# Performance work log

Measured on AMD Instinct MI355X. Metric: run time of the kernel, lower is better.

The kernel has to match this reference:

```python
import math
import jax, jax.numpy as jnp
import numpy as np

# ---- module hyperparameters (from init_kwargs) ----
N_DELTA, N_THETA, N_GAMMA = 32, 64, 256
N_TOTAL = N_DELTA + N_THETA + N_GAMMA  # 352
N_DIMS = 1024
BATCH = 4096
N_STEPS = 32
DT = 0.01
COUPLING = 2.0
PAC = 0.3
EPS = 1e-6
TWO_PI = 2.0 * math.pi


def setup_inputs() -> dict:
    key = jax.random.key(0)
    k0, k1, k2 = jax.random.split(key, 3)
    x = jax.random.normal(k0, (BATCH, N_DIMS), dtype=jnp.float32)
    # xavier_uniform with gain=0.5 for Linear(n_dims, n_total, bias=False)
    bound = 0.5 * math.sqrt(6.0 / (N_DIMS + N_TOTAL))
    W_phase = jax.random.uniform(k1, (N_TOTAL, N_DIMS), jnp.float32, -bound, bound)
    W_amp = jax.random.uniform(k2, (N_TOTAL, N_DIMS), jnp.float32, -bound, bound)
    # natural angular frequencies per band: delta ~2Hz, theta ~6Hz, gamma ~40Hz
    omega = jnp.concatenate([
        jnp.full((N_DELTA,), TWO_PI * 2.0, jnp.float32),
        jnp.full((N_THETA,), TWO_PI * 6.0, jnp.float32),
        jnp.full((N_GAMMA,), TWO_PI * 40.0, jnp.float32),
    ])
    # block-diagonal intra-band Kuramoto coupling, K_ij = coupling_strength / n_band
    Kn = np.zeros((N_TOTAL, N_TOTAL), dtype=np.float32)
    o = 0
    for nb in (N_DELTA, N_THETA, N_GAMMA):
        Kn[o:o + nb, o:o + nb] = COUPLING / nb
        o += nb
    K = jnp.asarray(Kn)
    return {"x": x, "W_phase": W_phase, "W_amp": W_amp, "omega": omega, "K": K}


def reference(x, W_phase, W_amp, omega, K):
    # learned projections -> initial phase in [0, 2pi), amplitude clamped >= eps
    phase0 = (x @ W_phase.T) % TWO_PI                      # (B, n_total)
    amp0 = jnp.maximum(jnp.abs(x @ W_amp.T), EPS)          # (B, n_total)

    def step(carry, _):
        phase, amp = carry
        s, c = jnp.sin(phase), jnp.cos(phase)
        # sum_j K_ij sin(phi_j - phi_i) = cos(phi_i)*(K@sin)_i - sin(phi_i)*(K@cos)_i
        coup = c * (s @ K.T) - s * (c @ K.T)
        phase_n = (phase + DT * (omega + coup)) % TWO_PI
        d = phase_n[:, :N_DELTA]
        t = phase_n[:, N_DELTA:N_DELTA + N_THETA]
        mean_d = jnp.arctan2(jnp.sin(d).mean(-1), jnp.cos(d).mean(-1))  # (B,)
        mean_t = jnp.arctan2(jnp.sin(t).mean(-1), jnp.cos(t).mean(-1))  # (B,)
        B = phase.shape[0]
        mod = jnp.concatenate([
            jnp.zeros((B, N_DELTA), phase.dtype),
            jnp.broadcast_to((PAC * jnp.cos(mean_d))[:, None], (B, N_THETA)),
            jnp.broadcast_to((PAC * jnp.cos(mean_t))[:, None], (B, N_GAMMA)),
        ], axis=-1)
        amp_n = jnp.maximum(amp * (1.0 + DT * mod), EPS)
        return (phase_n, amp_n), None

    (final_phase, final_amp), _ = jax.lax.scan(step, (phase0, amp0), None, length=N_STEPS)
    return final_amp
```

## Files before the change

kernel.cpp:

```cpp
#include <hip/hip_runtime.h>

typedef float  f32x4 __attribute__((ext_vector_type(4)));
typedef short  s16x8 __attribute__((ext_vector_type(8)));
typedef _Float16 h2 __attribute__((ext_vector_type(2)));
typedef unsigned short u16;
typedef u16 u16x4 __attribute__((ext_vector_type(4)));

#define N_DIMS 1024
#define N_OSC  352
#define BATCH  4096
#define EPSV   1e-6f
#define INV2PI 0.15915494309189535f

__device__ __forceinline__ u16 f2bf(float f){
  unsigned u = __builtin_bit_cast(unsigned, f);
  u += 0x7FFFu + ((u >> 16) & 1u);
  return (u16)(u >> 16);
}

#define NX4 1048576
#define NW4 90112

__global__ __launch_bounds__(256) void convert_k(const f32x4* __restrict__ x,
    const f32x4* __restrict__ wp, const f32x4* __restrict__ wa,
    u16x4* __restrict__ xb, u16x4* __restrict__ wb){
  int i = blockIdx.x * 256 + threadIdx.x;
  f32x4 v; u16x4* dst;
  if (i < NX4) { v = x[i]; dst = xb + i; }
  else {
    int j = i - NX4;
    v = (j < NW4) ? wp[j] : wa[j - NW4];
    dst = wb + j;
  }
  u16x4 r;
  r[0]=f2bf(v[0]); r[1]=f2bf(v[1]); r[2]=f2bf(v[2]); r[3]=f2bf(v[3]);
  *dst = r;
}

__device__ __forceinline__ void gload16(const u16* g, u16* l){
  __builtin_amdgcn_global_load_lds(
      (const __attribute__((address_space(1))) unsigned int*)(g),
      (__attribute__((address_space(3))) unsigned int*)(l), 16, 0, 0);
}

__global__ __launch_bounds__(256) void gemm_k(const u16* __restrict__ xb,
    const u16* __restrict__ wb, float* __restrict__ phase0, float* __restrict__ amp0){
  __shared__ u16 lds[2][8192];
  const int tid = threadIdx.x;
  const int l   = tid & 63;
  const int w   = tid >> 6;

  const int bid = blockIdx.x;
  const int xcd = bid & 7;
  const int r   = bid >> 3;
  const int mt  = xcd * 8 + r / 11;
  const int nt  = r % 11;
  const int m0  = mt * 64;
  const int n0  = nt * 64;

  const int srow = w*16 + (l >> 3);
  const int scol = (((l & 7) ^ (l >> 3)) * 8);
  const u16* ga = xb + (size_t)(m0 + srow) * N_DIMS + scol;
  const u16* gb = wb + (size_t)(n0 + srow) * N_DIMS + scol;

  #define STAGE(b, kt) { \
    const u16* gA = ga + (kt)*64; \
    const u16* gB = gb + (kt)*64; \
    gload16(gA,            &lds[b][w*1024]); \
    gload16(gA + 8*N_DIMS, &lds[b][w*1024 + 512]); \
    gload16(gB,            &lds[b][4096 + w*1024]); \
    gload16(gB + 8*N_DIMS, &lds[b][4096 + w*1024 + 512]); }

  const int rl = l & 15;
  const int q0 = l >> 4;
  const int sx = l & 7;
  const int wr = w >> 1, wc = w & 1;

  f32x4 acc[2][2] = {};
  STAGE(0, 0)
  __syncthreads();

  for (int kt = 0; kt < 16; kt++){
    const int cb = kt & 1;
    if (kt < 15) STAGE(cb^1, kt+1)
    s16x8 a[2][2], b[2][2];
    #pragma unroll
    for (int mi = 0; mi < 2; mi++)
    #pragma unroll
    for (int ks = 0; ks < 2; ks++){
      int off = (wr*32 + mi*16 + rl)*64 + (((ks*4 + q0) ^ sx) * 8);
      a[mi][ks] = *(const s16x8*)&lds[cb][off];
    }
    #pragma unroll
    for (int nj = 0; nj < 2; nj++)
    #pragma unroll
    for (int ks = 0; ks < 2; ks++){
      int off = 4096 + (wc*32 + nj*16 + rl)*64 + (((ks*4 + q0) ^ sx) * 8);
      b[nj][ks] = *(const s16x8*)&lds[cb][off];
    }
    #pragma unroll
    for (int ks = 0; ks < 2; ks++)
    #pragma unroll
    for (int mi = 0; mi < 2; mi++)
    #pragma unroll
    for (int nj = 0; nj < 2; nj++)
      acc[mi][nj] = __builtin_amdgcn_mfma_f32_16x16x32_bf16(a[mi][ks], b[nj][ks], acc[mi][nj], 0,0,0);
    __syncthreads();
  }
  #undef STAGE

  #pragma unroll
  for (int mi = 0; mi < 2; mi++)
  #pragma unroll
  for (int nj = 0; nj < 2; nj++){
    const int n = n0 + wc*32 + nj*16 + rl;
    #pragma unroll
    for (int rg = 0; rg < 4; rg++){
      const int m = m0 + wr*32 + mi*16 + q0*4 + rg;
      float v = acc[mi][nj][rg];
      if (n < N_OSC) { float t = v * INV2PI; phase0[(size_t)m*N_OSC + n] = t - floorf(t); }
      else           { amp0[(size_t)m*N_OSC + (n - N_OSC)] = fmaxf(fabsf(v), EPSV); }
    }
  }
}

__device__ __forceinline__ int ibc(h2 v){ return __builtin_bit_cast(int, v); }
__device__ __forceinline__ h2  hbc(int v){ return __builtin_bit_cast(h2, v); }

__device__ __forceinline__ h2 rowsum16(h2 x){
  int v = ibc(x);
  v = ibc(hbc(v) + hbc(__builtin_amdgcn_mov_dpp(v, 0x121, 0xF, 0xF, true)));
  v = ibc(hbc(v) + hbc(__builtin_amdgcn_mov_dpp(v, 0x122, 0xF, 0xF, true)));
  v = ibc(hbc(v) + hbc(__builtin_amdgcn_mov_dpp(v, 0x124, 0xF, 0xF, true)));
  v = ibc(hbc(v) + hbc(__builtin_amdgcn_mov_dpp(v, 0x128, 0xF, 0xF, true)));
  return hbc(v);
}

__device__ __forceinline__ void updp(h2& s, h2& c, h2 cA, h2 sA, h2 GS, h2 GC){
  h2 e  = c*GS - s*GC;
  h2 s1 = s*cA + c*sA;
  h2 c1 = c*cA - s*sA;
  s = s1 + c1*e;
  c = c1 - s1*e;
}

__device__ __forceinline__ h2 splat2(_Float16 v){ h2 r; r[0]=v; r[1]=v; return r; }

__global__ __launch_bounds__(256) void iter_k(const float* __restrict__ phase0,
                                              float* __restrict__ amp){
  const int tid = threadIdx.x;
  const int l   = tid & 63;
  const int g   = l & 15;
  const int row = blockIdx.x*16 + (tid>>6)*4 + (l>>4);
  const size_t rb = (size_t)row * N_OSC;

  const h2 cAd = splat2((_Float16)0.99211470f), sAd = splat2((_Float16)0.12533323f);
  const h2 cAt = splat2((_Float16)0.92977649f), sAt = splat2((_Float16)0.36812455f);
  const h2 cAg = splat2((_Float16)-0.80901699f), sAg = splat2((_Float16)0.58778525f);
  const h2 kd = splat2((_Float16)6.25e-4f);
  const h2 kt = splat2((_Float16)3.125e-4f);
  const h2 kg = splat2((_Float16)7.8125e-5f);

  h2 sD, cD, sT[2], cT[2], sG[8], cG[8];
  {
    const float* pr = phase0 + rb;
    #define SCP(dstS, dstC, idx, p0, p1) { \
      float a0 = (p0), a1 = (p1); \
      dstS[idx][0] = (_Float16)__builtin_amdgcn_sinf(a0); \
      dstS[idx][1] = (_Float16)__builtin_amdgcn_sinf(a1); \
      dstC[idx][0] = (_Float16)__builtin_amdgcn_cosf(a0); \
      dstC[idx][1] = (_Float16)__builtin_amdgcn_cosf(a1); }
    {
      float2 d = *(const float2*)(pr + 2*g);
      sD[0] = (_Float16)__builtin_amdgcn_sinf(d.x);
      sD[1] = (_Float16)__builtin_amdgcn_sinf(d.y);
      cD[0] = (_Float16)__builtin_amdgcn_cosf(d.x);
      cD[1] = (_Float16)__builtin_amdgcn_cosf(d.y);
    }
    {
      float4 t = *(const float4*)(pr + 32 + 4*g);
      SCP(sT, cT, 0, t.x, t.y) SCP(sT, cT, 1, t.z, t.w)
    }
    #pragma unroll
    for (int i = 0; i < 4; i++){
      float4 v = *(const float4*)(pr + 96 + 16*g + 4*i);
      SCP(sG, cG, 2*i,   v.x, v.y) SCP(sG, cG, 2*i+1, v.z, v.w)
    }
    #undef SCP
  }

  h2 PD, PT, PG;
  #define REDUCE { \
    h2 pd; pd[0] = sD[0]+sD[1]; pd[1] = cD[0]+cD[1]; \
    h2 ts = sT[0]+sT[1], tc = cT[0]+cT[1]; \
    h2 pt; pt[0] = ts[0]+ts[1]; pt[1] = tc[0]+tc[1]; \
    h2 gs = ((sG[0]+sG[1])+(sG[2]+sG[3]))+((sG[4]+sG[5])+(sG[6]+sG[7])); \
    h2 gc = ((cG[0]+cG[1])+(cG[2]+cG[3]))+((cG[4]+cG[5])+(cG[6]+cG[7])); \
    h2 pg; pg[0] = gs[0]+gs[1]; pg[1] = gc[0]+gc[1]; \
    PD = rowsum16(pd); PT = rowsum16(pt); PG = rowsum16(pg); }

  REDUCE

  float Pth = 1.f, Pga = 1.f, mPth = 1.f, mPga = 1.f;
  for (int t = 0; t < 32; t++){
    h2 gd = PD * kd, gt = PT * kt, gg = PG * kg;
    h2 GSd = splat2(gd[0]), GCd = splat2(gd[1]);
    h2 GSt = splat2(gt[0]), GCt = splat2(gt[1]);
    h2 GSg = splat2(gg[0]), GCg = splat2(gg[1]);
    updp(sD, cD, cAd, sAd, GSd, GCd);
    updp(sT[0], cT[0], cAt, sAt, GSt, GCt);
    updp(sT[1], cT[1], cAt, sAt, GSt, GCt);
    #pragma unroll
    for (int i = 0; i < 8; i++) updp(sG[i], cG[i], cAg, sAg, GSg, GCg);
    REDUCE
    float Sd = (float)PD[0], Cd = (float)PD[1];
    float St = (float)PT[0], Ct = (float)PT[1];
    float ft = 1.f + 0.003f * Cd * __builtin_amdgcn_rsqf(Cd*Cd + Sd*Sd);
    float fg = 1.f + 0.003f * Ct * __builtin_amdgcn_rsqf(Ct*Ct + St*St);
    Pth *= ft; mPth = fminf(mPth, Pth);
    Pga *= fg; mPga = fminf(mPga, Pga);
  }
  #undef REDUCE

  const float cth = EPSV * Pth / mPth;
  const float cga = EPSV * Pga / mPga;
  {
    float4 a = *(const float4*)(amp + rb + 32 + 4*g);
    a.x = fmaxf(a.x*Pth, cth); a.y = fmaxf(a.y*Pth, cth);
    a.z = fmaxf(a.z*Pth, cth); a.w = fmaxf(a.w*Pth, cth);
    *(float4*)(amp + rb + 32 + 4*g) = a;
  }
  #pragma unroll
  for (int i = 0; i < 4; i++){
    float4 a = *(const float4*)(amp + rb + 96 + 16*g + 4*i);
    a.x = fmaxf(a.x*Pga, cga); a.y = fmaxf(a.y*Pga, cga);
    a.z = fmaxf(a.z*Pga, cga); a.w = fmaxf(a.w*Pga, cga);
    *(float4*)(amp + rb + 96 + 16*g + 4*i) = a;
  }
}

extern "C" void kernel_launch(void* const* d_in, const int* in_sizes, int n_in,
                              void* d_out, int out_size, void* d_ws, size_t ws_size,
                              hipStream_t stream){
  const float* x  = (const float*)d_in[0];
  const float* wp = (const float*)d_in[1];
  const float* wa = (const float*)d_in[2];
  float* out = (float*)d_out;
  char* ws = (char*)d_ws;
  u16* xb  = (u16*)(ws);
  u16* wb  = (u16*)(ws + 8388608);
  float* phase0 = (float*)(ws + 9830400);

  convert_k<<<4800, 256, 0, stream>>>((const f32x4*)x, (const f32x4*)wp, (const f32x4*)wa,
                                      (u16x4*)xb, (u16x4*)wb);
  gemm_k<<<704, 256, 0, stream>>>(xb, wb, phase0, out);
  iter_k<<<256, 256, 0, stream>>>(phase0, out);
}
```

Before: 32.99 us.

## Split each oscillator row across 32 lanes with merged delta/theta lanes

The iteration kernel now gives each batch row 32 lanes instead of 16. Each lane holds 8 gamma oscillators, plus either 4 theta or 2 delta oscillators depending on its lane half. Gamma sums are reduced across 32 lanes using an extra ds_swizzle, and the delta/theta means are exchanged between half-waves. The grid doubles to 512 blocks to spread the serial 32-step recurrence over more lanes, at the cost of extra cross-lane swizzles per step and some idle work in the delta half.

```diff
diff --git a/kernel.cpp b/kernel.cpp
--- a/kernel.cpp
+++ b/kernel.cpp
@@ -126,15 +126,23 @@
 
 __device__ __forceinline__ int ibc(h2 v){ return __builtin_bit_cast(int, v); }
 __device__ __forceinline__ h2  hbc(int v){ return __builtin_bit_cast(h2, v); }
-
-__device__ __forceinline__ h2 rowsum16(h2 x){
-  int v = ibc(x);
-  v = ibc(hbc(v) + hbc(__builtin_amdgcn_mov_dpp(v, 0x121, 0xF, 0xF, true)));
-  v = ibc(hbc(v) + hbc(__builtin_amdgcn_mov_dpp(v, 0x122, 0xF, 0xF, true)));
-  v = ibc(hbc(v) + hbc(__builtin_amdgcn_mov_dpp(v, 0x124, 0xF, 0xF, true)));
-  v = ibc(hbc(v) + hbc(__builtin_amdgcn_mov_dpp(v, 0x128, 0xF, 0xF, true)));
-  return hbc(v);
-}
+__device__ __forceinline__ h2 splat2(_Float16 v){ h2 r; r[0]=v; r[1]=v; return r; }
+
+#define RED16(p) { \
+  int v_ = ibc(p); \
+  v_ = ibc(hbc(v_) + hbc(__builtin_amdgcn_mov_dpp(v_, 0x121, 0xF, 0xF, true))); \
+  v_ = ibc(hbc(v_) + hbc(__builtin_amdgcn_mov_dpp(v_, 0x122, 0xF, 0xF, true))); \
+  v_ = ibc(hbc(v_) + hbc(__builtin_amdgcn_mov_dpp(v_, 0x124, 0xF, 0xF, true))); \
+  v_ = ibc(hbc(v_) + hbc(__builtin_amdgcn_mov_dpp(v_, 0x128, 0xF, 0xF, true))); \
+  p = hbc(v_); }
+#define RED32(p) { \
+  int v_ = ibc(p); \
+  v_ = ibc(hbc(v_) + hbc(__builtin_amdgcn_mov_dpp(v_, 0x121, 0xF, 0xF, true))); \
+  v_ = ibc(hbc(v_) + hbc(__builtin_amdgcn_mov_dpp(v_, 0x122, 0xF, 0xF, true))); \
+  v_ = ibc(hbc(v_) + hbc(__builtin_amdgcn_mov_dpp(v_, 0x124, 0xF, 0xF, true))); \
+  v_ = ibc(hbc(v_) + hbc(__builtin_amdgcn_mov_dpp(v_, 0x128, 0xF, 0xF, true))); \
+  v_ = ibc(hbc(v_) + hbc(__builtin_amdgcn_ds_swizzle(v_, 0x401F))); \
+  p = hbc(v_); }
 
 __device__ __forceinline__ void updp(h2& s, h2& c, h2 cA, h2 sA, h2 GS, h2 GC){
   h2 e  = c*GS - s*GC;
@@ -144,77 +152,69 @@
   c = c1 - s1*e;
 }
 
-__device__ __forceinline__ h2 splat2(_Float16 v){ h2 r; r[0]=v; r[1]=v; return r; }
-
 __global__ __launch_bounds__(256) void iter_k(const float* __restrict__ phase0,
                                               float* __restrict__ amp){
   const int tid = threadIdx.x;
   const int l   = tid & 63;
-  const int g   = l & 15;
-  const int row = blockIdx.x*16 + (tid>>6)*4 + (l>>4);
+  const int j   = l & 31;
+  const bool lo16 = (j < 16);
+  const int row = blockIdx.x*8 + (tid>>6)*2 + (l>>5);
   const size_t rb = (size_t)row * N_OSC;
-
-  const h2 cAd = splat2((_Float16)0.99211470f), sAd = splat2((_Float16)0.12533323f);
-  const h2 cAt = splat2((_Float16)0.92977649f), sAt = splat2((_Float16)0.36812455f);
+  const float* pr = phase0 + rb;
+
   const h2 cAg = splat2((_Float16)-0.80901699f), sAg = splat2((_Float16)0.58778525f);
-  const h2 kd = splat2((_Float16)6.25e-4f);
-  const h2 kt = splat2((_Float16)3.125e-4f);
-  const h2 kg = splat2((_Float16)7.8125e-5f);
-
-  h2 sD, cD, sT[2], cT[2], sG[8], cG[8];
+  const h2 kg  = splat2((_Float16)7.8125e-5f);
+  const h2 cAe = lo16 ? splat2((_Float16)0.92977649f) : splat2((_Float16)0.99211470f);
+  const h2 sAe = lo16 ? splat2((_Float16)0.36812455f) : splat2((_Float16)0.12533323f);
+  const h2 ke  = lo16 ? splat2((_Float16)3.125e-4f)  : splat2((_Float16)6.25e-4f);
+
+  h2 sG[4], cG[4], sE[2], cE[2];
   {
-    const float* pr = phase0 + rb;
-    #define SCP(dstS, dstC, idx, p0, p1) { \
-      float a0 = (p0), a1 = (p1); \
-      dstS[idx][0] = (_Float16)__builtin_amdgcn_sinf(a0); \
-      dstS[idx][1] = (_Float16)__builtin_amdgcn_sinf(a1); \
-      dstC[idx][0] = (_Float16)__builtin_amdgcn_cosf(a0); \
-      dstC[idx][1] = (_Float16)__builtin_amdgcn_cosf(a1); }
-    {
-      float2 d = *(const float2*)(pr + 2*g);
-      sD[0] = (_Float16)__builtin_amdgcn_sinf(d.x);
-      sD[1] = (_Float16)__builtin_amdgcn_sinf(d.y);
-      cD[0] = (_Float16)__builtin_amdgcn_cosf(d.x);
-      cD[1] = (_Float16)__builtin_amdgcn_cosf(d.y);
-    }
-    {
-      float4 t = *(const float4*)(pr + 32 + 4*g);
-      SCP(sT, cT, 0, t.x, t.y) SCP(sT, cT, 1, t.z, t.w)
-    }
-    #pragma unroll
-    for (int i = 0; i < 4; i++){
-      float4 v = *(const float4*)(pr + 96 + 16*g + 4*i);
-      SCP(sG, cG, 2*i,   v.x, v.y) SCP(sG, cG, 2*i+1, v.z, v.w)
-    }
-    #undef SCP
-  }
-
-  h2 PD, PT, PG;
+    float4 g0 = *(const float4*)(pr + 96 + 8*j);
+    float4 g1 = *(const float4*)(pr + 96 + 8*j + 4);
+    float e0, e1, e2, e3;
+    if (lo16){ float4 t = *(const float4*)(pr + 32 + 4*j); e0=t.x; e1=t.y; e2=t.z; e3=t.w; }
+    else     { float2 d = *(const float2*)(pr + 2*(j-16)); e0=d.x; e1=d.y; e2=0.f; e3=0.f; }
+    #define SC2(dS, dC, i, p0, p1) { \
+      dS[i][0] = (_Float16)__builtin_amdgcn_sinf(p0); \
+      dS[i][1] = (_Float16)__builtin_amdgcn_sinf(p1); \
+      dC[i][0] = (_Float16)__builtin_amdgcn_cosf(p0); \
+      dC[i][1] = (_Float16)__builtin_amdgcn_cosf(p1); }
+    SC2(sG, cG, 0, g0.x, g0.y) SC2(sG, cG, 1, g0.z, g0.w)
+    SC2(sG, cG, 2, g1.x, g1.y) SC2(sG, cG, 3, g1.z, g1.w)
+    SC2(sE, cE, 0, e0, e1)     SC2(sE, cE, 1, e2, e3)
+    #undef SC2
+    if (!lo16){ sE[1] = splat2((_Float16)0.f); cE[1] = splat2((_Float16)0.f); }
+  }
+
+  h2 PG, PE;
   #define REDUCE { \
-    h2 pd; pd[0] = sD[0]+sD[1]; pd[1] = cD[0]+cD[1]; \
-    h2 ts = sT[0]+sT[1], tc = cT[0]+cT[1]; \
-    h2 pt; pt[0] = ts[0]+ts[1]; pt[1] = tc[0]+tc[1]; \
-    h2 gs = ((sG[0]+sG[1])+(sG[2]+sG[3]))+((sG[4]+sG[5])+(sG[6]+sG[7])); \
-    h2 gc = ((cG[0]+cG[1])+(cG[2]+cG[3]))+((cG[4]+cG[5])+(cG[6]+cG[7])); \
-    h2 pg; pg[0] = gs[0]+gs[1]; pg[1] = gc[0]+gc[1]; \
-    PD = rowsum16(pd); PT = rowsum16(pt); PG = rowsum16(pg); }
+    h2 sgp = (sG[0]+sG[1])+(sG[2]+sG[3]); \
+    h2 cgp = (cG[0]+cG[1])+(cG[2]+cG[3]); \
+    h2 pg; pg[0] = sgp[0]+sgp[1]; pg[1] = cgp[0]+cgp[1]; \
+    h2 sep = sE[0]+sE[1]; h2 cep = cE[0]+cE[1]; \
+    h2 pe; pe[0] = sep[0]+sep[1]; pe[1] = cep[0]+cep[1]; \
+    RED32(pg) RED16(pe) \
+    PG = pg; PE = pe; }
 
   REDUCE
 
   float Pth = 1.f, Pga = 1.f, mPth = 1.f, mPga = 1.f;
   for (int t = 0; t < 32; t++){
-    h2 gd = PD * kd, gt = PT * kt, gg = PG * kg;
-    h2 GSd = splat2(gd[0]), GCd = splat2(gd[1]);
-    h2 GSt = splat2(gt[0]), GCt = splat2(gt[1]);
+    h2 gg = PG * kg;
+    h2 ge = PE * ke;
     h2 GSg = splat2(gg[0]), GCg = splat2(gg[1]);
-    updp(sD, cD, cAd, sAd, GSd, GCd);
-    updp(sT[0], cT[0], cAt, sAt, GSt, GCt);
-    updp(sT[1], cT[1], cAt, sAt, GSt, GCt);
-    #pragma unroll
-    for (int i = 0; i < 8; i++) updp(sG[i], cG[i], cAg, sAg, GSg, GCg);
+    h2 GSe = splat2(ge[0]), GCe = splat2(ge[1]);
+    #pragma unroll
+    for (int i = 0; i < 4; i++) updp(sG[i], cG[i], cAg, sAg, GSg, GCg);
+    updp(sE[0], cE[0], cAe, sAe, GSe, GCe);
+    updp(sE[1], cE[1], cAe, sAe, GSe, GCe);
     REDUCE
-    float Sd = (float)PD[0], Cd = (float)PD[1];
-    float St = (float)PT[0], Ct = (float)PT[1];
+    h2 other = hbc(__builtin_amdgcn_ds_swizzle(ibc(PE), 0x401F));
+    h2 Th = lo16 ? PE : other;
+    h2 Dh = lo16 ? other : PE;
+    float Sd = (float)Dh[0], Cd = (float)Dh[1];
+    float St = (float)Th[0], Ct = (float)Th[1];
     float ft = 1.f + 0.003f * Cd * __builtin_amdgcn_rsqf(Cd*Cd + Sd*Sd);
     float fg = 1.f + 0.003f * Ct * __builtin_amdgcn_rsqf(Ct*Ct + St*St);
     Pth *= ft; mPth = fminf(mPth, Pth);
@@ -225,17 +225,20 @@
   const float cth = EPSV * Pth / mPth;
   const float cga = EPSV * Pga / mPga;
   {
-    float4 a = *(const float4*)(amp + rb + 32 + 4*g);
+    float4 a0 = *(const float4*)(amp + rb + 96 + 8*j);
+    a0.x = fmaxf(a0.x*Pga, cga); a0.y = fmaxf(a0.y*Pga, cga);
+    a0.z = fmaxf(a0.z*Pga, cga); a0.w = fmaxf(a0.w*Pga, cga);
+    *(float4*)(amp + rb + 96 + 8*j) = a0;
+    float4 a1 = *(const float4*)(amp + rb + 96 + 8*j + 4);
+    a1.x = fmaxf(a1.x*Pga, cga); a1.y = fmaxf(a1.y*Pga, cga);
+    a1.z = fmaxf(a1.z*Pga, cga); a1.w = fmaxf(a1.w*Pga, cga);
+    *(float4*)(amp + rb + 96 + 8*j + 4) = a1;
+  }
+  if (lo16){
+    float4 a = *(const float4*)(amp + rb + 32 + 4*j);
     a.x = fmaxf(a.x*Pth, cth); a.y = fmaxf(a.y*Pth, cth);
     a.z = fmaxf(a.z*Pth, cth); a.w = fmaxf(a.w*Pth, cth);
-    *(float4*)(amp + rb + 32 + 4*g) = a;
-  }
-  #pragma unroll
-  for (int i = 0; i < 4; i++){
-    float4 a = *(const float4*)(amp + rb + 96 + 16*g + 4*i);
-    a.x = fmaxf(a.x*Pga, cga); a.y = fmaxf(a.y*Pga, cga);
-    a.z = fmaxf(a.z*Pga, cga); a.w = fmaxf(a.w*Pga, cga);
-    *(float4*)(amp + rb + 96 + 16*g + 4*i) = a;
+    *(float4*)(amp + rb + 32 + 4*j) = a;
   }
 }
 
@@ -254,5 +257,5 @@
   convert_k<<<4800, 256, 0, stream>>>((const f32x4*)x, (const f32x4*)wp, (const f32x4*)wa,
                                       (u16x4*)xb, (u16x4*)wb);
   gemm_k<<<704, 256, 0, stream>>>(xb, wb, phase0, out);
-  iter_k<<<256, 256, 0, stream>>>(phase0, out);
-}
+  iter_k<<<512, 256, 0, stream>>>(phase0, out);
+}
```

Measured after the change: 33.43 us. Within noise of the previous version (+1.4%).

## Use single-wave 64x64 GEMM tiles with triple-buffered async loads and bf16 phase

Applied to the files above, without the earlier changes.

The GEMM block changes from four waves each computing 32x32 to one wave computing the whole 64x64 tile with a 4x4 MFMA accumulator. It uses a three-stage LDS ring driven by vmcnt waits instead of __syncthreads. The intermediate phase buffer is now stored as bf16, which halves that traffic, and iter_k decodes it. Risks are lower occupancy from fewer waves and more registers per block, and reduced phase precision.

```diff
diff --git a/kernel.cpp b/kernel.cpp
--- a/kernel.cpp
+++ b/kernel.cpp
@@ -16,6 +16,9 @@
   unsigned u = __builtin_bit_cast(unsigned, f);
   u += 0x7FFFu + ((u >> 16) & 1u);
   return (u16)(u >> 16);
+}
+__device__ __forceinline__ float bf2f(unsigned h){
+  return __builtin_bit_cast(float, h << 16);
 }
 
 #define NX4 1048576
@@ -43,12 +46,10 @@
       (__attribute__((address_space(3))) unsigned int*)(l), 16, 0, 0);
 }
 
-__global__ __launch_bounds__(256) void gemm_k(const u16* __restrict__ xb,
-    const u16* __restrict__ wb, float* __restrict__ phase0, float* __restrict__ amp0){
-  __shared__ u16 lds[2][8192];
-  const int tid = threadIdx.x;
-  const int l   = tid & 63;
-  const int w   = tid >> 6;
+__global__ __launch_bounds__(64) void gemm_k(const u16* __restrict__ xb,
+    const u16* __restrict__ wb, u16* __restrict__ phase0, float* __restrict__ amp0){
+  __shared__ u16 lds[3][8192];
+  const int l = threadIdx.x;
 
   const int bid = blockIdx.x;
   const int xcd = bid & 7;
@@ -58,68 +59,70 @@
   const int m0  = mt * 64;
   const int n0  = nt * 64;
 
-  const int srow = w*16 + (l >> 3);
-  const int scol = (((l & 7) ^ (l >> 3)) * 8);
+  const int srow = l >> 3;
+  const int scol = ((l & 7) ^ srow) * 8;
   const u16* ga = xb + (size_t)(m0 + srow) * N_DIMS + scol;
   const u16* gb = wb + (size_t)(n0 + srow) * N_DIMS + scol;
 
   #define STAGE(b, kt) { \
-    const u16* gA = ga + (kt)*64; \
-    const u16* gB = gb + (kt)*64; \
-    gload16(gA,            &lds[b][w*1024]); \
-    gload16(gA + 8*N_DIMS, &lds[b][w*1024 + 512]); \
-    gload16(gB,            &lds[b][4096 + w*1024]); \
-    gload16(gB + 8*N_DIMS, &lds[b][4096 + w*1024 + 512]); }
+    _Pragma("unroll") \
+    for (int i = 0; i < 8; i++){ \
+      gload16(ga + (kt)*64 + i*8*N_DIMS, &lds[b][i*512]); \
+      gload16(gb + (kt)*64 + i*8*N_DIMS, &lds[b][4096 + i*512]); } }
 
   const int rl = l & 15;
   const int q0 = l >> 4;
-  const int sx = l & 7;
-  const int wr = w >> 1, wc = w & 1;
-
-  f32x4 acc[2][2] = {};
+  const int sx = rl & 7;
+
+  f32x4 acc[4][4] = {};
+
+  #define COMPUTE(b) { \
+    s16x8 af[4][2], bf[4][2]; \
+    _Pragma("unroll") \
+    for (int mi = 0; mi < 4; mi++){ \
+      const int row = mi*16 + rl; \
+      af[mi][0] = *(const s16x8*)&lds[b][row*64 + ((q0 ^ sx) * 8)]; \
+      af[mi][1] = *(const s16x8*)&lds[b][row*64 + (((4 + q0) ^ sx) * 8)]; \
+    } \
+    _Pragma("unroll") \
+    for (int nj = 0; nj < 4; nj++){ \
+      const int row = nj*16 + rl; \
+      bf[nj][0] = *(const s16x8*)&lds[b][4096 + row*64 + ((q0 ^ sx) * 8)]; \
+      bf[nj][1] = *(const s16x8*)&lds[b][4096 + row*64 + (((4 + q0) ^ sx) * 8)]; \
+    } \
+    _Pragma("unroll") \
+    for (int ks = 0; ks < 2; ks++) \
+    _Pragma("unroll") \
+    for (int mi = 0; mi < 4; mi++) \
+    _Pragma("unroll") \
+    for (int nj = 0; nj < 4; nj++) \
+      acc[mi][nj] = __builtin_amdgcn_mfma_f32_16x16x32_bf16(af[mi][ks], bf[nj][ks], acc[mi][nj], 0,0,0); }
+
   STAGE(0, 0)
-  __syncthreads();
-
+  STAGE(1, 1)
+
+  #pragma unroll
   for (int kt = 0; kt < 16; kt++){
-    const int cb = kt & 1;
-    if (kt < 15) STAGE(cb^1, kt+1)
-    s16x8 a[2][2], b[2][2];
+    if (kt < 15) asm volatile("s_waitcnt vmcnt(16)" ::: "memory");
+    else         asm volatile("s_waitcnt vmcnt(0)"  ::: "memory");
+    COMPUTE(kt % 3)
+    if (kt < 14) STAGE((kt + 2) % 3, kt + 2)
+  }
+  #undef STAGE
+  #undef COMPUTE
+
+  #pragma unroll
+  for (int nj = 0; nj < 4; nj++){
+    const int n = n0 + nj*16 + rl;
+    const bool isph = (n < N_OSC);
     #pragma unroll
-    for (int mi = 0; mi < 2; mi++)
-    #pragma unroll
-    for (int ks = 0; ks < 2; ks++){
-      int off = (wr*32 + mi*16 + rl)*64 + (((ks*4 + q0) ^ sx) * 8);
-      a[mi][ks] = *(const s16x8*)&lds[cb][off];
-    }
-    #pragma unroll
-    for (int nj = 0; nj < 2; nj++)
-    #pragma unroll
-    for (int ks = 0; ks < 2; ks++){
-      int off = 4096 + (wc*32 + nj*16 + rl)*64 + (((ks*4 + q0) ^ sx) * 8);
-      b[nj][ks] = *(const s16x8*)&lds[cb][off];
-    }
-    #pragma unroll
-    for (int ks = 0; ks < 2; ks++)
-    #pragma unroll
-    for (int mi = 0; mi < 2; mi++)
-    #pragma unroll
-    for (int nj = 0; nj < 2; nj++)
-      acc[mi][nj] = __builtin_amdgcn_mfma_f32_16x16x32_bf16(a[mi][ks], b[nj][ks], acc[mi][nj], 0,0,0);
-    __syncthreads();
-  }
-  #undef STAGE
-
-  #pragma unroll
-  for (int mi = 0; mi < 2; mi++)
-  #pragma unroll
-  for (int nj = 0; nj < 2; nj++){
-    const int n = n0 + wc*32 + nj*16 + rl;
+    for (int mi = 0; mi < 4; mi++)
     #pragma unroll
     for (int rg = 0; rg < 4; rg++){
-      const int m = m0 + wr*32 + mi*16 + q0*4 + rg;
+      const int m = m0 + mi*16 + q0*4 + rg;
       float v = acc[mi][nj][rg];
-      if (n < N_OSC) { float t = v * INV2PI; phase0[(size_t)m*N_OSC + n] = t - floorf(t); }
-      else           { amp0[(size_t)m*N_OSC + (n - N_OSC)] = fmaxf(fabsf(v), EPSV); }
+      if (isph){ float t = v * INV2PI; t -= floorf(t); phase0[(size_t)m*N_OSC + n] = f2bf(t); }
+      else     { amp0[(size_t)m*N_OSC + (n - N_OSC)] = fmaxf(fabsf(v), EPSV); }
     }
   }
 }
@@ -146,7 +149,7 @@
 
 __device__ __forceinline__ h2 splat2(_Float16 v){ h2 r; r[0]=v; r[1]=v; return r; }
 
-__global__ __launch_bounds__(256) void iter_k(const float* __restrict__ phase0,
+__global__ __launch_bounds__(256) void iter_k(const u16* __restrict__ phase0,
                                               float* __restrict__ amp){
   const int tid = threadIdx.x;
   const int l   = tid & 63;
@@ -163,30 +166,34 @@
 
   h2 sD, cD, sT[2], cT[2], sG[8], cG[8];
   {
-    const float* pr = phase0 + rb;
-    #define SCP(dstS, dstC, idx, p0, p1) { \
-      float a0 = (p0), a1 = (p1); \
-      dstS[idx][0] = (_Float16)__builtin_amdgcn_sinf(a0); \
-      dstS[idx][1] = (_Float16)__builtin_amdgcn_sinf(a1); \
-      dstC[idx][0] = (_Float16)__builtin_amdgcn_cosf(a0); \
-      dstC[idx][1] = (_Float16)__builtin_amdgcn_cosf(a1); }
+    const u16* pr = phase0 + rb;
+    unsigned dw = *(const unsigned*)(pr + 2*g);
+    uint2 tw    = *(const uint2*)(pr + 32 + 4*g);
+    uint4 g0w   = *(const uint4*)(pr + 96 + 16*g);
+    uint4 g1w   = *(const uint4*)(pr + 96 + 16*g + 8);
+    #define SC2(dS, dC, i, p0, p1) { \
+      dS[i][0] = (_Float16)__builtin_amdgcn_sinf(p0); \
+      dS[i][1] = (_Float16)__builtin_amdgcn_sinf(p1); \
+      dC[i][0] = (_Float16)__builtin_amdgcn_cosf(p0); \
+      dC[i][1] = (_Float16)__builtin_amdgcn_cosf(p1); }
     {
-      float2 d = *(const float2*)(pr + 2*g);
-      sD[0] = (_Float16)__builtin_amdgcn_sinf(d.x);
-      sD[1] = (_Float16)__builtin_amdgcn_sinf(d.y);
-      cD[0] = (_Float16)__builtin_amdgcn_cosf(d.x);
-      cD[1] = (_Float16)__builtin_amdgcn_cosf(d.y);
+      float d0 = bf2f(dw & 0xFFFFu), d1 = bf2f(dw >> 16);
+      sD[0] = (_Float16)__builtin_amdgcn_sinf(d0);
+      sD[1] = (_Float16)__builtin_amdgcn_sinf(d1);
+      cD[0] = (_Float16)__builtin_amdgcn_cosf(d0);
+      cD[1] = (_Float16)__builtin_amdgcn_cosf(d1);
     }
-    {
-      float4 t = *(const float4*)(pr + 32 + 4*g);
-      SCP(sT, cT, 0, t.x, t.y) SCP(sT, cT, 1, t.z, t.w)
-    }
-    #pragma unroll
-    for (int i = 0; i < 4; i++){
-      float4 v = *(const float4*)(pr + 96 + 16*g + 4*i);
-      SCP(sG, cG, 2*i,   v.x, v.y) SCP(sG, cG, 2*i+1, v.z, v.w)
-    }
-    #undef SCP
+    SC2(sT, cT, 0, bf2f(tw.x & 0xFFFFu), bf2f(tw.x >> 16))
+    SC2(sT, cT, 1, bf2f(tw.y & 0xFFFFu), bf2f(tw.y >> 16))
+    SC2(sG, cG, 0, bf2f(g0w.x & 0xFFFFu), bf2f(g0w.x >> 16))
+    SC2(sG, cG, 1, bf2f(g0w.y & 0xFFFFu), bf2f(g0w.y >> 16))
+    SC2(sG, cG, 2, bf2f(g0w.z & 0xFFFFu), bf2f(g0w.z >> 16))
+    SC2(sG, cG, 3, bf2f(g0w.w & 0xFFFFu), bf2f(g0w.w >> 16))
+    SC2(sG, cG, 4, bf2f(g1w.x & 0xFFFFu), bf2f(g1w.x >> 16))
+    SC2(sG, cG, 5, bf2f(g1w.y & 0xFFFFu), bf2f(g1w.y >> 16))
+    SC2(sG, cG, 6, bf2f(g1w.z & 0xFFFFu), bf2f(g1w.z >> 16))
+    SC2(sG, cG, 7, bf2f(g1w.w & 0xFFFFu), bf2f(g1w.w >> 16))
+    #undef SC2
   }
 
   h2 PD, PT, PG;
@@ -249,10 +256,10 @@
   char* ws = (char*)d_ws;
   u16* xb  = (u16*)(ws);
   u16* wb  = (u16*)(ws + 8388608);
-  float* phase0 = (float*)(ws + 9830400);
+  u16* phase0 = (u16*)(ws + 9830400);
 
   convert_k<<<4800, 256, 0, stream>>>((const f32x4*)x, (const f32x4*)wp, (const f32x4*)wa,
                                       (u16x4*)xb, (u16x4*)wb);
-  gemm_k<<<704, 256, 0, stream>>>(xb, wb, phase0, out);
+  gemm_k<<<704, 64, 0, stream>>>(xb, wb, phase0, out);
   iter_k<<<256, 256, 0, stream>>>(phase0, out);
 }
```

Measured after the change: 36.78 us. +11.5%, slower.
